# Optimization experiments

Hardware: AMD Instinct MI355X
Metric: run time of the kernel (lower is better)

The kernel has to match this reference:

```python
import jax, jax.numpy as jnp
import numpy as np

B, C_IN, MID, H, W = 4, 512, 512, 50, 50
A = 9
FEAT_STRIDE = 16
IMG = H * FEAT_STRIDE  # 800
N_PRE, N_POST = 1200, 300
NMS_TH = 0.7
MIN_SIZE = 16.0


def _anchor_base(base=16.0, ratios=(0.5, 1.0, 2.0), scales=(8, 16, 32)):
    ab = np.zeros((len(ratios) * len(scales), 4), np.float32)
    py = px = base / 2.0
    for i, r in enumerate(ratios):
        for j, s in enumerate(scales):
            h = base * s * np.sqrt(r)
            w = base * s * np.sqrt(1.0 / r)
            ab[i * len(scales) + j] = [py - h / 2, px - w / 2, py + h / 2, px + w / 2]
    return ab


def _all_anchors():
    ab = _anchor_base()
    sy = np.arange(0, H * FEAT_STRIDE, FEAT_STRIDE, dtype=np.float32)
    sx = np.arange(0, W * FEAT_STRIDE, FEAT_STRIDE, dtype=np.float32)
    SX, SY = np.meshgrid(sx, sy)
    shift = np.stack([SY.ravel(), SX.ravel(), SY.ravel(), SX.ravel()], axis=1)
    return jnp.asarray((shift[:, None, :] + ab[None]).reshape(-1, 4))  # [H*W*A,4]


ANCHORS = _all_anchors()


def _conv(x, w, b, pad):
    y = jax.lax.conv_general_dilated(x, w, (1, 1), [(pad, pad), (pad, pad)],
                                     dimension_numbers=('NCHW', 'OIHW', 'NCHW'))
    return y + b[None, :, None, None]


def _loc2bbox(anc, loc):
    h = anc[:, 2] - anc[:, 0]
    w = anc[:, 3] - anc[:, 1]
    cy = anc[:, 0] + 0.5 * h
    cx = anc[:, 1] + 0.5 * w
    dy, dx, dh, dw = loc[:, 0], loc[:, 1], loc[:, 2], loc[:, 3]
    ncy = dy * h + cy
    ncx = dx * w + cx
    nh = jnp.exp(dh) * h
    nw = jnp.exp(dw) * w
    return jnp.stack([ncy - 0.5 * nh, ncx - 0.5 * nw, ncy + 0.5 * nh, ncx + 0.5 * nw], axis=1)


def _nms_keep(boxes, thresh):
    y1, x1, y2, x2 = boxes[:, 0], boxes[:, 1], boxes[:, 2], boxes[:, 3]
    iy = jnp.clip(jnp.minimum(y2[:, None], y2[None]) - jnp.maximum(y1[:, None], y1[None]), 0.0)
    ix = jnp.clip(jnp.minimum(x2[:, None], x2[None]) - jnp.maximum(x1[:, None], x1[None]), 0.0)
    inter = iy * ix
    area = (y2 - y1) * (x2 - x1)
    iou = inter / (area[:, None] + area[None] - inter + 1e-9)  # [N_PRE,N_PRE]

    def step(carry, i):
        sup, keep = carry
        k = ~sup[i]
        keep = keep.at[i].set(k)
        newsup = jnp.where(k & (iou[i] > thresh), True, sup)
        newsup = newsup.at[i].set(sup[i])
        return (newsup, keep), None

    n = boxes.shape[0]
    init = (jnp.zeros(n, bool), jnp.zeros(n, bool))
    (_, keep), _ = jax.lax.scan(step, init, jnp.arange(n))
    return keep


def _propose(loc, fg):
    roi = _loc2bbox(ANCHORS, loc)
    roi = jnp.stack([jnp.clip(roi[:, 0], 0.0, IMG), jnp.clip(roi[:, 1], 0.0, IMG),
                     jnp.clip(roi[:, 2], 0.0, IMG), jnp.clip(roi[:, 3], 0.0, IMG)], axis=1)
    hs = roi[:, 2] - roi[:, 0]
    ws = roi[:, 3] - roi[:, 1]
    s = jnp.where((hs >= MIN_SIZE) & (ws >= MIN_SIZE), fg, -jnp.inf)
    top_s, top_i = jax.lax.top_k(s, N_PRE)          # score-sorted pre-NMS candidates
    boxes = roi[top_i]
    keep = _nms_keep(boxes, NMS_TH)
    _, sel = jax.lax.top_k(jnp.where(keep, top_s, -jnp.inf), N_POST)
    return boxes[sel]                                # [N_POST,4]


def setup_inputs() -> dict:
    key = jax.random.key(0)
    ks = jax.random.split(key, 4)
    x = jax.random.normal(ks[0], (B, C_IN, H, W), jnp.float32)
    W1 = jax.random.normal(ks[1], (MID, C_IN, 3, 3), jnp.float32) * 0.01
    b1 = jnp.zeros((MID,), jnp.float32)
    Wl = jax.random.normal(ks[2], (A * 4, MID, 1, 1), jnp.float32) * 0.01
    bl = jnp.zeros((A * 4,), jnp.float32)
    Ws = jax.random.normal(ks[3], (A * 2, MID, 1, 1), jnp.float32) * 0.01
    bs = jnp.zeros((A * 2,), jnp.float32)
    return {'x': x, 'W1': W1, 'b1': b1, 'Wl': Wl, 'bl': bl, 'Ws': Ws, 'bs': bs}


def reference(x, W1, b1, Wl, bl, Ws, bs):
    h = jax.nn.relu(_conv(x, W1, b1, 1))
    locs = _conv(h, Wl, bl, 0)     # [B, A*4, H, W]
    scores = _conv(h, Ws, bs, 0)   # [B, A*2, H, W]
    rpn_locs = locs.transpose(0, 2, 3, 1).reshape(B, -1, 4)          # [B, H*W*A, 4]
    sc = scores.transpose(0, 2, 3, 1).reshape(B, H, W, A, 2)
    fg = jax.nn.softmax(sc, axis=-1)[..., 1].reshape(B, -1)          # [B, H*W*A]
    rpn_scores = sc.reshape(B, -1, 2)
    rois = jax.vmap(_propose)(rpn_locs, fg)                          # [B, N_POST, 4]
    return rpn_locs, rpn_scores, rois
```

## Files before the change

kernel.cpp:

```cpp
#include <hip/hip_runtime.h>
#include <math.h>

#define BATCH 4
#define CIN 512
#define MID 512
#define HH 50
#define WW 50
#define HWPIX 2500
#define NPIX 10000
#define NANCH 22500
#define NPRE 1200
#define NPOST 300
#define LOCS_OFF 0
#define SCORES_OFF 360000
#define ROIS_OFF 540000

#define PADW 52
#define PPIX 2704

typedef _Float16 half8 __attribute__((ext_vector_type(8)));
typedef float floatx4 __attribute__((ext_vector_type(4)));

__device__ __forceinline__ void gload16(const void* g, void* l) {
    __builtin_amdgcn_global_load_lds(
        (const __attribute__((address_space(1))) unsigned int*)g,
        (__attribute__((address_space(3))) unsigned int*)l, 16, 0, 0);
}

__device__ __forceinline__ unsigned long long rdlane64(unsigned int lo,
                                                       unsigned int hi, int l) {
    const unsigned int a = (unsigned int)__builtin_amdgcn_readlane((int)lo, l);
    const unsigned int b = (unsigned int)__builtin_amdgcn_readlane((int)hi, l);
    return ((unsigned long long)b << 32) | a;
}


__global__ __launch_bounds__(256) void prep_combo_kernel(
    const float* __restrict__ x, const float* __restrict__ W1,
    const float* __restrict__ Wl, const float* __restrict__ Wsc,
    _Float16* __restrict__ xh, _Float16* __restrict__ xl,
    _Float16* __restrict__ wth, _Float16* __restrict__ wtl,
    float* __restrict__ wh) {
    __shared__ __align__(16) char smem[18432];
    const int blk = blockIdx.x;
    const int t   = threadIdx.x;

    if (blk < 1280) {
        float (*tile)[65] = (float(*)[65])smem;
        const int pt = blk % 40;
        const int ct = (blk / 40) % 8;
        const int b  = blk / 320;
        const int p0 = pt * 64, c0 = ct * 64;

        #pragma unroll
        for (int r = 0; r < 16; ++r) {
            const int cc = (t >> 6) + r * 4;
            const int pp = t & 63;
            const int p  = p0 + pp;
            tile[cc][pp] = (p < HWPIX) ? x[((size_t)b * 512 + c0 + cc) * HWPIX + p] : 0.f;
        }
        __syncthreads();
        #pragma unroll
        for (int r = 0; r < 16; ++r) {
            const int pp = (t >> 6) + r * 4;
            const int cc = t & 63;
            const int p  = p0 + pp;
            if (p < HWPIX) {
                const int y = p / WW, xx2 = p % WW;
                const float v = tile[cc][pp];
                const _Float16 hh = (_Float16)v;
                const float rr = v - (float)hh;
                const _Float16 ll = (_Float16)(rr * 2048.0f);
                const size_t o = ((size_t)(b * PPIX + (y + 1) * PADW + xx2 + 1)) * 512 + c0 + cc;
                xh[o] = hh;
                xl[o] = ll;
            }
        }
    } else {
        const int wblk = blk - 1280;
        if (wblk < 512) {
            float* buf = (float*)smem;
            const int m = wblk;
            const float* src = W1 + (size_t)m * 4608;
            for (int i = t; i < 4608; i += 256) buf[i] = src[i];
            __syncthreads();
            for (int kk = 0; kk < 9; ++kk) {
                for (int c = t; c < 512; c += 256) {
                    const float v = buf[c * 9 + kk];
                    const _Float16 hh = (_Float16)v;
                    const float rr = v - (float)hh;
                    const size_t o = (size_t)kk * 262144 + (size_t)m * 512 + c;
                    wth[o] = hh;
                    wtl[o] = (_Float16)(rr * 2048.0f);
                }
            }
        } else if (wblk < 640) {
            const int g2 = (wblk - 512) * 256 + t;
            const int c = g2 >> 6, n = g2 & 63;
            float v = 0.f;
            if (n < 36)      v = Wl[n * 512 + c];
            else if (n < 54) v = Wsc[(n - 36) * 512 + c];
            wh[g2] = v;
        } else {
            const int idx = (wblk - 640) * 256 + t;
            if (idx < BATCH * PPIX * 4) {
                const int pix = idx >> 2, q = idx & 3;
                const int r = pix % PPIX;
                const int yy = r / PADW, xx2 = r % PADW;
                if (yy == 0 || yy == PADW - 1 || xx2 == 0 || xx2 == PADW - 1) {
                    float4 z = make_float4(0.f, 0.f, 0.f, 0.f);
                    float4* ph = (float4*)(xh + (size_t)pix * 512 + q * 128);
                    float4* pl = (float4*)(xl + (size_t)pix * 512 + q * 128);
                    #pragma unroll
                    for (int i = 0; i < 16; ++i) { ph[i] = z; pl[i] = z; }
                }
            }
        }
    }
}

#define BUFSZ 24576
#define AOFF_L 8192
#define BOFF_H 16384
#define BOFF_L 20480
#define MTILES 80

__global__ __launch_bounds__(256) void conv_mfma_kernel(
    const _Float16* __restrict__ xh, const _Float16* __restrict__ xl,
    const _Float16* __restrict__ wth, const _Float16* __restrict__ wtl,
    float* __restrict__ hp, int ksplit) {
    __shared__ __align__(16) char lds[2 * BUFSZ];

    const int bid  = blockIdx.x;
    const int t    = threadIdx.x;
    const int w    = t >> 6;
    const int lane = t & 63;
    const int m0   = (bid % MTILES) * 128;
    const int rr_  = bid / MTILES;
    int n0, s0, send, kh;
    if (ksplit) { n0 = (rr_ >> 1) * 64; kh = rr_ & 1; s0 = kh * 72; send = s0 + 72; }
    else        { n0 = rr_ * 64;        kh = 0;       s0 = 0;       send = 144; }
    float* hout = hp + (size_t)kh * 5120000;
    const int wq   = w * 1024;

    const int sr = t >> 2;
    const int cp = t & 3;
    const int clA = (cp - (sr >> 1)) & 3;
    const int clB = clA;

    int P0 = m0 + sr;       if (P0 > NPIX - 1) P0 = NPIX - 1;
    int P1 = m0 + sr + 64;  if (P1 > NPIX - 1) P1 = NPIX - 1;
    const int b0 = P0 / HWPIX, pl0 = P0 % HWPIX;
    const int b1i = P1 / HWPIX, pl1 = P1 % HWPIX;
    const int baseA0 = ((b0 * PPIX) + (pl0 / WW + 1) * PADW + (pl0 % WW + 1)) * 512 + clA * 8;
    const int baseA1 = ((b1i * PPIX) + (pl1 / WW + 1) * PADW + (pl1 % WW + 1)) * 512 + clA * 8;
    const int baseB  = (n0 + sr) * 512 + clB * 8;

    const int lr = lane & 15, lq = lane >> 4;
    const int wrow = w * 32;
    const int rA0 = wrow + lr, rA1 = wrow + 16 + lr;
    const int offA0 = rA0 * 64 + (((lq + (rA0 >> 1)) & 3) << 4);
    const int offA1 = rA1 * 64 + (((lq + (rA1 >> 1)) & 3) << 4);
    int offB[4];
    #pragma unroll
    for (int ctl = 0; ctl < 4; ++ctl) {
        const int rB = ctl * 16 + lr;
        offB[ctl] = rB * 64 + (((lq + (rB >> 1)) & 3) << 4);
    }

    floatx4 acc1[2][4] = {};
    floatx4 acc2[2][4] = {};

    auto issue = [&](int u) {
        char* D = lds + ((u & 1) ? BUFSZ : 0);
        const int kk = u >> 4, ct = u & 15;
        const int kd = kk / 3;
        const int dA = ((kd - 1) * PADW + (kk - kd * 3 - 1)) * 512 + ct * 32;
        const int dB = kk * 262144 + ct * 32;
        gload16(xh + baseA0 + dA, D + 0 + wq);
        gload16(xh + baseA1 + dA, D + 4096 + wq);
        gload16(xl + baseA0 + dA, D + AOFF_L + wq);
        gload16(xl + baseA1 + dA, D + AOFF_L + 4096 + wq);
        gload16(wth + baseB + dB, D + BOFF_H + wq);
        gload16(wtl + baseB + dB, D + BOFF_L + wq);
    };

    issue(s0);
    for (int s = s0; s < send; ++s) {
        __syncthreads();
        if (s + 1 < send) issue(s + 1);
        const char* Bb = lds + ((s & 1) ? BUFSZ : 0);
        const half8 afh0 = *(const half8*)(Bb + offA0);
        const half8 afh1 = *(const half8*)(Bb + offA1);
        const half8 afl0 = *(const half8*)(Bb + AOFF_L + offA0);
        const half8 afl1 = *(const half8*)(Bb + AOFF_L + offA1);
        #pragma unroll
        for (int ctl = 0; ctl < 4; ++ctl) {
            const half8 bfh = *(const half8*)(Bb + BOFF_H + offB[ctl]);
            const half8 bfl = *(const half8*)(Bb + BOFF_L + offB[ctl]);
            acc1[0][ctl] = __builtin_amdgcn_mfma_f32_16x16x32_f16(afh0, bfh, acc1[0][ctl], 0, 0, 0);
            acc2[0][ctl] = __builtin_amdgcn_mfma_f32_16x16x32_f16(afh0, bfl, acc2[0][ctl], 0, 0, 0);
            acc2[0][ctl] = __builtin_amdgcn_mfma_f32_16x16x32_f16(afl0, bfh, acc2[0][ctl], 0, 0, 0);
            acc1[1][ctl] = __builtin_amdgcn_mfma_f32_16x16x32_f16(afh1, bfh, acc1[1][ctl], 0, 0, 0);
            acc2[1][ctl] = __builtin_amdgcn_mfma_f32_16x16x32_f16(afh1, bfl, acc2[1][ctl], 0, 0, 0);
            acc2[1][ctl] = __builtin_amdgcn_mfma_f32_16x16x32_f16(afl1, bfh, acc2[1][ctl], 0, 0, 0);
        }
    }

    const float s2 = 1.0f / 2048.0f;
    #pragma unroll
    for (int rt = 0; rt < 2; ++rt) {
        #pragma unroll
        for (int ctl = 0; ctl < 4; ++ctl) {
            const int m = n0 + ctl * 16 + lr;
            #pragma unroll
            for (int r = 0; r < 4; ++r) {
                const int P = m0 + wrow + rt * 16 + lq * 4 + r;
                if (P < NPIX)
                    hout[(size_t)P * 512 + m] = acc1[rt][ctl][r] + acc2[rt][ctl][r] * s2;
            }
        }
    }
}

__global__ void wt_kernel(const float* __restrict__ W1,
                          const float* __restrict__ Wl,
                          const float* __restrict__ Wsc,
                          float* __restrict__ w1t, float* __restrict__ wh) {
    int g = blockIdx.x * 256 + threadIdx.x;
    if (g < 9 * 512 * 512) {
        int kk = g / (512 * 512);
        int r  = g % (512 * 512);
        int c  = r / 512;
        int m  = r % 512;
        w1t[g] = W1[(size_t)m * 4608 + c * 9 + kk];
    } else {
        int g2 = g - 9 * 512 * 512;
        if (g2 < 512 * 64) {
            int c = g2 >> 6, n = g2 & 63;
            float v = 0.f;
            if (n < 36)      v = Wl[n * 512 + c];
            else if (n < 54) v = Wsc[(n - 36) * 512 + c];
            wh[g2] = v;
        }
    }
}

__global__ __launch_bounds__(256) void conv3x3_fallback(
    const float* __restrict__ x, const float* __restrict__ w1t,
    float* __restrict__ h) {
    __shared__ float As[16][64];
    __shared__ float Bs[16][64];
    const int t  = threadIdx.x;
    const int tx = t & 15;
    const int ty = t >> 4;
    const int m0 = blockIdx.x * 64;
    const int n0 = blockIdx.y * 64;
    const int pix = t & 63;
    const int cl0 = t >> 6;
    const int P  = m0 + pix;
    const bool vp = (P < NPIX);
    const int b  = P / HWPIX;
    const int pl = P % HWPIX;
    const int yy = pl / WW;
    const int xx = pl % WW;
    float acc[4][4] = {};
    for (int kk = 0; kk < 9; ++kk) {
        const int ky = kk / 3 - 1, kx = kk % 3 - 1;
        const int y2 = yy + ky, x2 = xx + kx;
        const bool v = vp && ((unsigned)y2 < (unsigned)HH) && ((unsigned)x2 < (unsigned)WW);
        const float* xbase = x + (size_t)b * CIN * HWPIX + y2 * WW + x2;
        const float* wbase = w1t + (size_t)kk * 512 * 512 + n0;
        for (int ct = 0; ct < 512 / 16; ++ct) {
            __syncthreads();
            #pragma unroll
            for (int r = 0; r < 4; ++r) {
                const int cl = cl0 + r * 4;
                const int c  = ct * 16 + cl;
                As[cl][pix] = v ? xbase[(size_t)c * HWPIX] : 0.f;
                Bs[cl][pix] = wbase[c * 512 + pix];
            }
            __syncthreads();
            #pragma unroll
            for (int k = 0; k < 16; ++k) {
                const float4 a4 = *reinterpret_cast<const float4*>(&As[k][ty * 4]);
                const float4 b4 = *reinterpret_cast<const float4*>(&Bs[k][tx * 4]);
                const float av[4] = {a4.x, a4.y, a4.z, a4.w};
                const float bv[4] = {b4.x, b4.y, b4.z, b4.w};
                #pragma unroll
                for (int i = 0; i < 4; ++i)
                    #pragma unroll
                    for (int j = 0; j < 4; ++j)
                        acc[i][j] = fmaf(av[i], bv[j], acc[i][j]);
            }
        }
    }
    #pragma unroll
    for (int i = 0; i < 4; ++i) {
        const int Pp = m0 + ty * 4 + i;
        if (Pp >= NPIX) continue;
        const int m = n0 + tx * 4;
        float4 o;
        o.x = acc[i][0];
        o.y = acc[i][1];
        o.z = acc[i][2];
        o.w = acc[i][3];
        *reinterpret_cast<float4*>(&h[(size_t)Pp * 512 + m]) = o;
    }
}


__global__ __launch_bounds__(256) void heads_kernel(
    const float* __restrict__ h0, const float* __restrict__ h1,
    const float* __restrict__ wh, const float* __restrict__ b1,
    const float* __restrict__ bl, const float* __restrict__ bsc,
    float* __restrict__ out, float* __restrict__ roi_all,
    unsigned long long* __restrict__ keys) {
    #pragma clang fp contract(off)
    __shared__ float As[16][17];
    __shared__ float Bs[16][64];
    __shared__ float fgs[16][9];
    const int t  = threadIdx.x;
    const int p  = t & 15;
    const int g  = t >> 4;
    const int p0 = blockIdx.x * 16;

    float acc[4] = {0.f, 0.f, 0.f, 0.f};

    for (int ct = 0; ct < 32; ++ct) {
        const int c0 = ct * 16;
        __syncthreads();
        {
            const int pp = t >> 4, cc = t & 15;
            const int PP = p0 + pp;
            float v = 0.f;
            if (PP < NPIX) {
                const size_t o = (size_t)PP * 512 + c0 + cc;
                v = h0[o];
                if (h1) v += h1[o];
                v = fmaxf(v + b1[c0 + cc], 0.f);
            }
            As[cc][pp] = v;
            #pragma unroll
            for (int r = 0; r < 4; ++r) {
                const int row = (t >> 6) + 4 * r;
                Bs[row][t & 63] = wh[(size_t)(c0 + row) * 64 + (t & 63)];
            }
        }
        __syncthreads();
        #pragma unroll
        for (int k = 0; k < 16; ++k) {
            const float a = As[k][p];
            const float4 b4 = *reinterpret_cast<const float4*>(&Bs[k][g * 4]);
            acc[0] = fmaf(a, b4.x, acc[0]);
            acc[1] = fmaf(a, b4.y, acc[1]);
            acc[2] = fmaf(a, b4.z, acc[2]);
            acc[3] = fmaf(a, b4.w, acc[3]);
        }
    }

    const int P  = p0 + p;
    const int b  = (P < NPIX) ? (P / HWPIX) : 0;
    const int pl = (P < NPIX) ? (P % HWPIX) : 0;
    const int n  = g * 4;
    const size_t abase = (size_t)b * NANCH + (size_t)pl * 9;
    const bool vP = (P < NPIX);

    float4 locv = make_float4(0.f, 0.f, 0.f, 0.f);
    if (vP && n < 36) {
        locv.x = acc[0] + bl[n + 0];
        locv.y = acc[1] + bl[n + 1];
        locv.z = acc[2] + bl[n + 2];
        locv.w = acc[3] + bl[n + 3];
        *reinterpret_cast<float4*>(&out[LOCS_OFF + (abase + g) * 4]) = locv;
    } else if (vP && n < 54) {
        const int ns = n - 36;
        float* so = out + SCORES_OFF;
        {
            const float s0 = acc[0] + bsc[ns + 0];
            const float s1 = acc[1] + bsc[ns + 1];
            const int a0 = ns >> 1;
            so[(abase + a0) * 2 + 0] = s0;
            so[(abase + a0) * 2 + 1] = s1;
            const float mx = fmaxf(s0, s1);
            const float e0 = expf(s0 - mx);
            const float e1 = expf(s1 - mx);
            fgs[p][a0] = e1 / (e0 + e1);
        }
        if (ns + 3 < 18) {
            const float s0 = acc[2] + bsc[ns + 2];
            const float s1 = acc[3] + bsc[ns + 3];
            const int a1 = (ns >> 1) + 1;
            so[(abase + a1) * 2 + 0] = s0;
            so[(abase + a1) * 2 + 1] = s1;
            const float mx = fmaxf(s0, s1);
            const float e0 = expf(s0 - mx);
            const float e1 = expf(s1 - mx);
            fgs[p][a1] = e1 / (e0 + e1);
        }
    }
    __syncthreads();

    if (vP && n < 36) {
        const int a = g;
        const int j = pl * 9 + a;
        const int y = pl / WW;
        const int x = pl % WW;
        const int ri = a / 3, si = a % 3;
        const double rrd[3] = {0.5, 1.0, 2.0};
        const double ssd[3] = {8.0, 16.0, 32.0};
        const double hh = 16.0 * ssd[si] * sqrt(rrd[ri]);
        const double wd = 16.0 * ssd[si] * sqrt(1.0 / rrd[ri]);
        const float ab0 = (float)(8.0 - hh / 2.0);
        const float ab1 = (float)(8.0 - wd / 2.0);
        const float ab2 = (float)(8.0 + hh / 2.0);
        const float ab3 = (float)(8.0 + wd / 2.0);
        const float sy = (float)(y * 16);
        const float sx = (float)(x * 16);
        const float ay1 = sy + ab0;
        const float ax1 = sx + ab1;
        const float ay2 = sy + ab2;
        const float ax2 = sx + ab3;

        const float h  = ay2 - ay1;
        const float w  = ax2 - ax1;
        const float cy = ay1 + 0.5f * h;
        const float cx = ax1 + 0.5f * w;

        const float dy = locv.x, dx = locv.y, dh = locv.z, dw = locv.w;
        const float ncy = dy * h + cy;
        const float ncx = dx * w + cx;
        const float nh  = expf(dh) * h;
        const float nw  = expf(dw) * w;

        float r0 = ncy - 0.5f * nh;
        float r1 = ncx - 0.5f * nw;
        float r2 = ncy + 0.5f * nh;
        float r3 = ncx + 0.5f * nw;
        r0 = fminf(fmaxf(r0, 0.f), 800.f);
        r1 = fminf(fmaxf(r1, 0.f), 800.f);
        r2 = fminf(fmaxf(r2, 0.f), 800.f);
        r3 = fminf(fmaxf(r3, 0.f), 800.f);

        const float hs  = r2 - r0;
        const float wsz = r3 - r1;
        const float fg  = fgs[p][a];
        const float s   = (hs >= 16.f && wsz >= 16.f) ? fg : -__builtin_huge_valf();

        float4 ro;
        ro.x = r0; ro.y = r1; ro.z = r2; ro.w = r3;
        *reinterpret_cast<float4*>(&roi_all[((size_t)b * NANCH + j) * 4]) = ro;

        unsigned int bits = __float_as_uint(s);
        unsigned int o = (bits & 0x80000000u) ? ~bits : (bits | 0x80000000u);
        keys[(size_t)b * NANCH + j] =
            ((unsigned long long)o << 32) | (unsigned int)(~(unsigned int)j);
    }
}

__global__ __launch_bounds__(1024) void select_sort_kernel(
    const unsigned long long* __restrict__ keys,
    const float* __restrict__ roi_all, float* __restrict__ boxes) {
    const int b   = blockIdx.x;
    const int tid = threadIdx.x;
    const unsigned long long* K = keys + (size_t)b * NANCH;

    __shared__ unsigned int hist[256][4];
    __shared__ unsigned int suf[256];
    __shared__ unsigned long long sbuf[2048];
    __shared__ unsigned int prefix_s;
    __shared__ int rank_s;
    __shared__ int cnt_s;

    const int sub = (tid >> 8) & 3;

    if (tid == 0) { prefix_s = 0u; rank_s = NPRE; }
    __syncthreads();

    for (int pass = 0; pass < 4; ++pass) {
        for (int i = tid; i < 1024; i += 1024) ((unsigned int*)hist)[i] = 0;
        __syncthreads();
        const unsigned pref = prefix_s;
        for (int i = tid; i < NANCH; i += 1024) {
            const unsigned hk = (unsigned)(K[i] >> 32);
            const bool match = (pass == 0) || ((hk >> (32 - 8 * pass)) == pref);
            if (match) atomicAdd(&hist[(hk >> (24 - 8 * pass)) & 255u][sub], 1u);
        }
        __syncthreads();
        if (tid < 256)
            suf[tid] = hist[tid][0] + hist[tid][1] + hist[tid][2] + hist[tid][3];
        __syncthreads();
        for (int st = 1; st < 256; st <<= 1) {
            unsigned v = 0;
            if (tid < 256) v = suf[tid] + ((tid + st < 256) ? suf[tid + st] : 0u);
            __syncthreads();
            if (tid < 256) suf[tid] = v;
            __syncthreads();
        }
        const int r = rank_s;
        __syncthreads();
        if (tid < 256) {
            const unsigned s_here = suf[tid];
            const unsigned s_up   = (tid < 255) ? suf[tid + 1] : 0u;
            if (s_here >= (unsigned)r && s_up < (unsigned)r) {
                rank_s = r - (int)s_up;
                prefix_s = (prefix_s << 8) | (unsigned)tid;
            }
        }
        __syncthreads();
    }

    const unsigned kth32 = prefix_s;
    if (tid == 0) cnt_s = 0;
    __syncthreads();
    for (int i = tid; i < NANCH; i += 1024) {
        const unsigned long long k = K[i];
        if ((unsigned)(k >> 32) >= kth32) {
            const int p = atomicAdd(&cnt_s, 1);
            if (p < 2048) sbuf[p] = k;
        }
    }
    __syncthreads();
    const int cnt = cnt_s;
    for (int i = tid; i < 2048; i += 1024)
        if (i >= cnt) sbuf[i] = 0ULL;

    for (int ksz = 2; ksz <= 2048; ksz <<= 1) {
        for (int jj = ksz >> 1; jj > 0; jj >>= 1) {
            __syncthreads();
            for (int i = tid; i < 2048; i += 1024) {
                const int l = i ^ jj;
                if (l > i) {
                    const unsigned long long a = sbuf[i];
                    const unsigned long long c = sbuf[l];
                    const bool asc = (i & ksz) != 0;
                    const bool sw  = asc ? (a > c) : (a < c);
                    if (sw) { sbuf[i] = c; sbuf[l] = a; }
                }
            }
        }
    }
    __syncthreads();

    for (int r = tid; r < NPRE; r += 1024) {
        const unsigned long long k = sbuf[r];
        const unsigned int idx = ~((unsigned int)k);
        const float4 v = *reinterpret_cast<const float4*>(
            &roi_all[((size_t)b * NANCH + idx) * 4]);
        *reinterpret_cast<float4*>(&boxes[((size_t)b * NPRE + r) * 4]) = v;
    }
}

__global__ __launch_bounds__(64) void iou_kernel(
    const float* __restrict__ boxes, unsigned long long* __restrict__ mask) {
    #pragma clang fp contract(off)
    const int rb = blockIdx.x;
    const int b  = blockIdx.y;
    const int t  = threadIdx.x;
    __shared__ float bx[NPRE * 4];
    __shared__ float ar[NPRE];

    for (int i = t; i < NPRE * 4; i += 64)
        bx[i] = boxes[(size_t)b * NPRE * 4 + i];
    __syncthreads();
    for (int i = t; i < NPRE; i += 64)
        ar[i] = (bx[i * 4 + 2] - bx[i * 4 + 0]) * (bx[i * 4 + 3] - bx[i * 4 + 1]);
    __syncthreads();

    const int i = rb * 64 + t;
    if (i >= NPRE) return;
    const float y1 = bx[i * 4 + 0], x1 = bx[i * 4 + 1];
    const float y2 = bx[i * 4 + 2], x2 = bx[i * 4 + 3];
    const float ai = ar[i];
    for (int jw = 0; jw < 19; ++jw) {
        unsigned long long bits = 0ULL;
        const int jmax = (jw * 64 + 64 <= NPRE) ? 64 : (NPRE - jw * 64);
        for (int jb = 0; jb < jmax; ++jb) {
            const int j = jw * 64 + jb;
            const float iy = fmaxf(fminf(y2, bx[j * 4 + 2]) - fmaxf(y1, bx[j * 4 + 0]), 0.f);
            const float ix = fmaxf(fminf(x2, bx[j * 4 + 3]) - fmaxf(x1, bx[j * 4 + 1]), 0.f);
            const float inter = iy * ix;
            const float den = ((ai + ar[j]) - inter) + 1e-9f;
            const float iou = inter / den;
            if (iou > 0.7f) bits |= (1ULL << jb);
        }
        mask[((size_t)b * NPRE + i) * 19 + jw] = bits;
    }
}

__global__ __launch_bounds__(64) void nms_scan_kernel(
    const unsigned long long* __restrict__ mask,
    const float* __restrict__ boxes, float* __restrict__ out_rois) {
    const int b    = blockIdx.x;
    const int lane = threadIdx.x;
    const unsigned long long* M = mask + (size_t)b * NPRE * 19;

    __shared__ unsigned long long tile[2][1216];
    __shared__ unsigned long long kw[19];
    __shared__ int sel[NPOST];

    const int lw = (lane < 19) ? lane : 0;

    {
        unsigned long long pre[19];
        #pragma unroll
        for (int q = 0; q < 19; ++q) pre[q] = M[q * 64 + lane];
        #pragma unroll
        for (int q = 0; q < 19; ++q) tile[0][q * 64 + lane] = pre[q];
    }
    __syncthreads();

    unsigned long long sup = 0ULL;

    for (int w = 0; w < 19; ++w) {
        const int cur = w & 1;
        unsigned long long pre[19];
        if (w + 1 < 19) {
            const int gb = (w + 1) * 1216;
            #pragma unroll
            for (int q = 0; q < 19; ++q) pre[q] = M[gb + q * 64 + lane];
        }

        const int nrows = (w == 18) ? (NPRE - 18 * 64) : 64;
        const unsigned long long* tp = tile[cur];

        const unsigned long long diag = (lane < nrows) ? tp[lane * 19 + w] : 0ULL;
        const unsigned int dlo = (unsigned int)diag;
        const unsigned int dhi = (unsigned int)(diag >> 32);

        const unsigned long long ext =
            rdlane64((unsigned int)sup, (unsigned int)(sup >> 32), w);

        unsigned long long sup_in = ext, keep = 0ULL;
        for (int i = 0; i < nrows; ++i) {
            const unsigned long long di = rdlane64(dlo, dhi, i);
            if (!((sup_in >> i) & 1ULL)) {
                keep |= (1ULL << i);
                sup_in |= di;
            }
        }

        #pragma unroll
        for (int i = 0; i < 64; ++i) {
            const unsigned long long mi = tp[i * 19 + lw];
            sup |= mi & (0ULL - ((keep >> i) & 1ULL));
        }

        if (lane == 0) kw[w] = keep;

        if (w + 1 < 19) {
            #pragma unroll
            for (int q = 0; q < 19; ++q) tile[1 - cur][q * 64 + lane] = pre[q];
        }
        __syncthreads();
    }

    int total = 0;
    #pragma unroll
    for (int w = 0; w < 19; ++w) total += __popcll(kw[w]);

    int pref = 0;
    #pragma unroll
    for (int w = 0; w < 19; ++w) {
        const unsigned long long kwv = kw[w];
        const int i = w * 64 + lane;
        const int kr = pref + __popcll(kwv & ((1ULL << lane) - 1ULL));
        if (i < NPRE) {
            if ((kwv >> lane) & 1ULL) {
                if (kr < NPOST) sel[kr] = i;
            } else {
                const int r2 = total + (i - kr);
                if (r2 < NPOST) sel[r2] = i;
            }
        }
        pref += __popcll(kwv);
    }
    __syncthreads();

    for (int rr = lane; rr < NPOST; rr += 64) {
        const int i = sel[rr];
        const float4 v = *reinterpret_cast<const float4*>(
            &boxes[((size_t)b * NPRE + i) * 4]);
        *reinterpret_cast<float4*>(&out_rois[((size_t)b * NPOST + rr) * 4]) = v;
    }
}

extern "C" void kernel_launch(void* const* d_in, const int* in_sizes, int n_in,
                              void* d_out, int out_size, void* d_ws, size_t ws_size,
                              hipStream_t stream) {
    const float* x   = (const float*)d_in[0];
    const float* W1  = (const float*)d_in[1];
    const float* b1  = (const float*)d_in[2];
    const float* Wl  = (const float*)d_in[3];
    const float* bl  = (const float*)d_in[4];
    const float* Wsc = (const float*)d_in[5];
    const float* bsc = (const float*)d_in[6];
    float* out = (float*)d_out;
    char* ws = (char*)d_ws;

    const size_t T_A = 72679424ULL;
    const size_t T_B = 52199424ULL;

    if (ws_size >= T_B) {
        const bool ksplit = (ws_size >= T_A);
        float*    h0;
        float*    h1 = nullptr;
        _Float16 *xh, *xl, *wth, *wtl;
        float*    wh;
        char*     alias;
        if (ksplit) {
            h0  = (float*)(ws);
            h1  = (float*)(ws + 20480000);
            xh  = (_Float16*)(ws + 40960000);
            xl  = (_Float16*)(ws + 52035584);
            wth = (_Float16*)(ws + 63111168);
            wtl = (_Float16*)(ws + 67829760);
            wh  = (float*)(ws + 72548352);
            alias = ws + 40960000;
        } else {
            h0  = (float*)(ws);
            xh  = (_Float16*)(ws + 20480000);
            xl  = (_Float16*)(ws + 31555584);
            wth = (_Float16*)(ws + 42631168);
            wtl = (_Float16*)(ws + 47349760);
            wh  = (float*)(ws + 52068352);
            alias = ws + 20480000;
        }
        float* roi   = (float*)(alias);
        unsigned long long* keys = (unsigned long long*)(alias + 1440000);
        float* boxes = (float*)(alias + 2160000);
        unsigned long long* mask = (unsigned long long*)(alias + 2236800);

        hipLaunchKernelGGL(prep_combo_kernel, dim3(1280 + 512 + 128 + 169), dim3(256), 0, stream,
                           x, W1, Wl, Wsc, xh, xl, wth, wtl, wh);
        hipLaunchKernelGGL(conv_mfma_kernel, dim3((ksplit ? 16 : 8) * MTILES), dim3(256), 0, stream,
                           xh, xl, wth, wtl, h0, (int)(ksplit ? 1 : 0));
        hipLaunchKernelGGL(heads_kernel, dim3(625), dim3(256), 0, stream,
                           h0, h1, wh, b1, bl, bsc, out, roi, keys);
        hipLaunchKernelGGL(select_sort_kernel, dim3(BATCH), dim3(1024), 0, stream,
                           keys, roi, boxes);
        hipLaunchKernelGGL(iou_kernel, dim3(19, BATCH), dim3(64), 0, stream,
                           boxes, mask);
        hipLaunchKernelGGL(nms_scan_kernel, dim3(BATCH), dim3(64), 0, stream,
                           mask, boxes, out + ROIS_OFF);
    } else {
        float* w1t = (float*)(ws);
        float* h   = (float*)(ws + 9437184);
        float* wh  = (float*)(ws + 29917184);
        float* roi = (float*)(ws + 30048256);
        unsigned long long* keys = (unsigned long long*)(ws + 31488256);
        float* boxes = (float*)(ws + 32208256);
        unsigned long long* mask = (unsigned long long*)(ws + 32285056);

        hipLaunchKernelGGL(wt_kernel, dim3((9 * 512 * 512 + 512 * 64 + 255) / 256),
                           dim3(256), 0, stream, W1, Wl, Wsc, w1t, wh);
        hipLaunchKernelGGL(conv3x3_fallback, dim3((NPIX + 63) / 64, 512 / 64), dim3(256), 0, stream,
                           x, w1t, h);
        hipLaunchKernelGGL(heads_kernel, dim3(625), dim3(256), 0, stream,
                           h, (const float*)nullptr, wh, b1, bl, bsc, out, roi, keys);
        hipLaunchKernelGGL(select_sort_kernel, dim3(BATCH), dim3(1024), 0, stream,
                           keys, roi, boxes);
        hipLaunchKernelGGL(iou_kernel, dim3(19, BATCH), dim3(64), 0, stream,
                           boxes, mask);
        hipLaunchKernelGGL(nms_scan_kernel, dim3(BATCH), dim3(64), 0, stream,
                           mask, boxes, out + ROIS_OFF);
    }
}
```

Before: 540.6 us.

## Fuse top-k sort, IoU mask and NMS scan into one kernel; vectorize fp16 split stores

Merges the select/sort, IoU-mask and NMS-scan kernels into a single per-batch 1024-thread kernel. Sorted boxes stay in shared memory instead of round-tripping through global memory, which removes two kernel launches. In exchange, the IoU computation now runs on only 4 workgroups rather than 76, which concentrates that work on a few compute units. The prep kernel also packs pairs of fp16 hi/lo values into half2 stores to cut store instruction count.

```diff
diff --git a/kernel.cpp b/kernel.cpp
--- a/kernel.cpp
+++ b/kernel.cpp
@@ -19,6 +19,7 @@
 #define PPIX 2704
 
 typedef _Float16 half8 __attribute__((ext_vector_type(8)));
+typedef _Float16 half2v __attribute__((ext_vector_type(2)));
 typedef float floatx4 __attribute__((ext_vector_type(4)));
 
 __device__ __forceinline__ void gload16(const void* g, void* l) {
@@ -61,19 +62,23 @@
         }
         __syncthreads();
         #pragma unroll
-        for (int r = 0; r < 16; ++r) {
-            const int pp = (t >> 6) + r * 4;
-            const int cc = t & 63;
-            const int p  = p0 + pp;
+        for (int r = 0; r < 8; ++r) {
+            const int pp  = (t >> 5) + r * 8;
+            const int cc2 = (t & 31) * 2;
+            const int p   = p0 + pp;
             if (p < HWPIX) {
                 const int y = p / WW, xx2 = p % WW;
-                const float v = tile[cc][pp];
-                const _Float16 hh = (_Float16)v;
-                const float rr = v - (float)hh;
-                const _Float16 ll = (_Float16)(rr * 2048.0f);
-                const size_t o = ((size_t)(b * PPIX + (y + 1) * PADW + xx2 + 1)) * 512 + c0 + cc;
-                xh[o] = hh;
-                xl[o] = ll;
+                const float v0 = tile[cc2][pp];
+                const float v1 = tile[cc2 + 1][pp];
+                const _Float16 h0 = (_Float16)v0;
+                const _Float16 l0 = (_Float16)((v0 - (float)h0) * 2048.0f);
+                const _Float16 h1 = (_Float16)v1;
+                const _Float16 l1 = (_Float16)((v1 - (float)h1) * 2048.0f);
+                const size_t o = ((size_t)(b * PPIX + (y + 1) * PADW + xx2 + 1)) * 512 + c0 + cc2;
+                half2v hv; hv[0] = h0; hv[1] = h1;
+                half2v lv; lv[0] = l0; lv[1] = l1;
+                *reinterpret_cast<half2v*>(xh + o) = hv;
+                *reinterpret_cast<half2v*>(xl + o) = lv;
             }
         }
     } else {
@@ -84,15 +89,19 @@
             const float* src = W1 + (size_t)m * 4608;
             for (int i = t; i < 4608; i += 256) buf[i] = src[i];
             __syncthreads();
+            const int c = t * 2;
             for (int kk = 0; kk < 9; ++kk) {
-                for (int c = t; c < 512; c += 256) {
-                    const float v = buf[c * 9 + kk];
-                    const _Float16 hh = (_Float16)v;
-                    const float rr = v - (float)hh;
-                    const size_t o = (size_t)kk * 262144 + (size_t)m * 512 + c;
-                    wth[o] = hh;
-                    wtl[o] = (_Float16)(rr * 2048.0f);
-                }
+                const float v0 = buf[c * 9 + kk];
+                const float v1 = buf[(c + 1) * 9 + kk];
+                const _Float16 h0 = (_Float16)v0;
+                const _Float16 l0 = (_Float16)((v0 - (float)h0) * 2048.0f);
+                const _Float16 h1 = (_Float16)v1;
+                const _Float16 l1 = (_Float16)((v1 - (float)h1) * 2048.0f);
+                const size_t o = (size_t)kk * 262144 + (size_t)m * 512 + c;
+                half2v hv; hv[0] = h0; hv[1] = h1;
+                half2v lv; lv[0] = l0; lv[1] = l1;
+                *reinterpret_cast<half2v*>(wth + o) = hv;
+                *reinterpret_cast<half2v*>(wtl + o) = lv;
             }
         } else if (wblk < 640) {
             const int g2 = (wblk - 512) * 256 + t;
@@ -458,27 +467,37 @@
     }
 }
 
-__global__ __launch_bounds__(1024) void select_sort_kernel(
-    const unsigned long long* __restrict__ keys,
-    const float* __restrict__ roi_all, float* __restrict__ boxes) {
+__global__ __launch_bounds__(1024) void postproc_kernel(
+    const unsigned long long* __restrict__ keys_g,
+    const float* __restrict__ roi_all,
+    unsigned long long* __restrict__ mask_g,
+    float* __restrict__ out_rois) {
+    #pragma clang fp contract(off)
     const int b   = blockIdx.x;
     const int tid = threadIdx.x;
-    const unsigned long long* K = keys + (size_t)b * NANCH;
-
-    __shared__ unsigned int hist[256][4];
-    __shared__ unsigned int suf[256];
-    __shared__ unsigned long long sbuf[2048];
+    const unsigned long long* K = keys_g + (size_t)b * NANCH;
+
+    __shared__ __align__(16) char arena[49152];
+    __shared__ unsigned long long kw[19];
+    __shared__ int sel[NPOST];
     __shared__ unsigned int prefix_s;
     __shared__ int rank_s;
     __shared__ int cnt_s;
 
+    unsigned int (*hist)[4]   = (unsigned int(*)[4])(arena);
+    unsigned int* suf         = (unsigned int*)(arena + 4096);
+    unsigned long long* sbuf  = (unsigned long long*)(arena + 8192);
+    float* bx                 = (float*)(arena + 24576);
+    float* ar                 = (float*)(arena + 43776);
+    unsigned long long* tileb = (unsigned long long*)(arena);
+
     const int sub = (tid >> 8) & 3;
 
     if (tid == 0) { prefix_s = 0u; rank_s = NPRE; }
     __syncthreads();
 
     for (int pass = 0; pass < 4; ++pass) {
-        for (int i = tid; i < 1024; i += 1024) ((unsigned int*)hist)[i] = 0;
+        ((unsigned int*)hist)[tid] = 0;
         __syncthreads();
         const unsigned pref = prefix_s;
         for (int i = tid; i < NANCH; i += 1024) {
@@ -547,58 +566,36 @@
         const unsigned int idx = ~((unsigned int)k);
         const float4 v = *reinterpret_cast<const float4*>(
             &roi_all[((size_t)b * NANCH + idx) * 4]);
-        *reinterpret_cast<float4*>(&boxes[((size_t)b * NPRE + r) * 4]) = v;
-    }
-}
-
-__global__ __launch_bounds__(64) void iou_kernel(
-    const float* __restrict__ boxes, unsigned long long* __restrict__ mask) {
-    #pragma clang fp contract(off)
-    const int rb = blockIdx.x;
-    const int b  = blockIdx.y;
-    const int t  = threadIdx.x;
-    __shared__ float bx[NPRE * 4];
-    __shared__ float ar[NPRE];
-
-    for (int i = t; i < NPRE * 4; i += 64)
-        bx[i] = boxes[(size_t)b * NPRE * 4 + i];
-    __syncthreads();
-    for (int i = t; i < NPRE; i += 64)
+        *reinterpret_cast<float4*>(&bx[r * 4]) = v;
+    }
+    __syncthreads();
+    for (int i = tid; i < NPRE; i += 1024)
         ar[i] = (bx[i * 4 + 2] - bx[i * 4 + 0]) * (bx[i * 4 + 3] - bx[i * 4 + 1]);
     __syncthreads();
 
-    const int i = rb * 64 + t;
-    if (i >= NPRE) return;
-    const float y1 = bx[i * 4 + 0], x1 = bx[i * 4 + 1];
-    const float y2 = bx[i * 4 + 2], x2 = bx[i * 4 + 3];
-    const float ai = ar[i];
-    for (int jw = 0; jw < 19; ++jw) {
-        unsigned long long bits = 0ULL;
-        const int jmax = (jw * 64 + 64 <= NPRE) ? 64 : (NPRE - jw * 64);
-        for (int jb = 0; jb < jmax; ++jb) {
-            const int j = jw * 64 + jb;
-            const float iy = fmaxf(fminf(y2, bx[j * 4 + 2]) - fmaxf(y1, bx[j * 4 + 0]), 0.f);
-            const float ix = fmaxf(fminf(x2, bx[j * 4 + 3]) - fmaxf(x1, bx[j * 4 + 1]), 0.f);
-            const float inter = iy * ix;
-            const float den = ((ai + ar[j]) - inter) + 1e-9f;
-            const float iou = inter / den;
-            if (iou > 0.7f) bits |= (1ULL << jb);
-        }
-        mask[((size_t)b * NPRE + i) * 19 + jw] = bits;
-    }
-}
-
-__global__ __launch_bounds__(64) void nms_scan_kernel(
-    const unsigned long long* __restrict__ mask,
-    const float* __restrict__ boxes, float* __restrict__ out_rois) {
-    const int b    = blockIdx.x;
-    const int lane = threadIdx.x;
-    const unsigned long long* M = mask + (size_t)b * NPRE * 19;
-
-    __shared__ unsigned long long tile[2][1216];
-    __shared__ unsigned long long kw[19];
-    __shared__ int sel[NPOST];
-
+    for (int i = tid; i < NPRE; i += 1024) {
+        const float y1 = bx[i * 4 + 0], x1 = bx[i * 4 + 1];
+        const float y2 = bx[i * 4 + 2], x2 = bx[i * 4 + 3];
+        const float ai = ar[i];
+        for (int jw = 0; jw < 19; ++jw) {
+            unsigned long long bits = 0ULL;
+            const int jmax = (jw * 64 + 64 <= NPRE) ? 64 : (NPRE - jw * 64);
+            for (int jb = 0; jb < jmax; ++jb) {
+                const int j = jw * 64 + jb;
+                const float iy = fmaxf(fminf(y2, bx[j * 4 + 2]) - fmaxf(y1, bx[j * 4 + 0]), 0.f);
+                const float ix = fmaxf(fminf(x2, bx[j * 4 + 3]) - fmaxf(x1, bx[j * 4 + 1]), 0.f);
+                const float inter = iy * ix;
+                const float den = ((ai + ar[j]) - inter) + 1e-9f;
+                const float iou = inter / den;
+                if (iou > 0.7f) bits |= (1ULL << jb);
+            }
+            mask_g[((size_t)b * NPRE + i) * 19 + jw] = bits;
+        }
+    }
+    __syncthreads();
+
+    const unsigned long long* M = mask_g + (size_t)b * NPRE * 19;
+    const int lane = tid & 63;
     const int lw = (lane < 19) ? lane : 0;
 
     {
@@ -606,7 +603,7 @@
         #pragma unroll
         for (int q = 0; q < 19; ++q) pre[q] = M[q * 64 + lane];
         #pragma unroll
-        for (int q = 0; q < 19; ++q) tile[0][q * 64 + lane] = pre[q];
+        for (int q = 0; q < 19; ++q) tileb[q * 64 + lane] = pre[q];
     }
     __syncthreads();
 
@@ -622,7 +619,7 @@
         }
 
         const int nrows = (w == 18) ? (NPRE - 18 * 64) : 64;
-        const unsigned long long* tp = tile[cur];
+        const unsigned long long* tp = tileb + cur * 1216;
 
         const unsigned long long diag = (lane < nrows) ? tp[lane * 19 + w] : 0ULL;
         const unsigned int dlo = (unsigned int)diag;
@@ -650,7 +647,7 @@
 
         if (w + 1 < 19) {
             #pragma unroll
-            for (int q = 0; q < 19; ++q) tile[1 - cur][q * 64 + lane] = pre[q];
+            for (int q = 0; q < 19; ++q) tileb[(1 - cur) * 1216 + q * 64 + lane] = pre[q];
         }
         __syncthreads();
     }
@@ -677,11 +674,12 @@
     }
     __syncthreads();
 
-    for (int rr = lane; rr < NPOST; rr += 64) {
-        const int i = sel[rr];
-        const float4 v = *reinterpret_cast<const float4*>(
-            &boxes[((size_t)b * NPRE + i) * 4]);
-        *reinterpret_cast<float4*>(&out_rois[((size_t)b * NPOST + rr) * 4]) = v;
+    if (tid < 64) {
+        for (int rr = tid; rr < NPOST; rr += 64) {
+            const int i = sel[rr];
+            const float4 v = *reinterpret_cast<const float4*>(&bx[i * 4]);
+            *reinterpret_cast<float4*>(&out_rois[((size_t)b * NPOST + rr) * 4]) = v;
+        }
     }
 }
 
@@ -728,8 +726,7 @@
         }
         float* roi   = (float*)(alias);
         unsigned long long* keys = (unsigned long long*)(alias + 1440000);
-        float* boxes = (float*)(alias + 2160000);
-        unsigned long long* mask = (unsigned long long*)(alias + 2236800);
+        unsigned long long* mask = (unsigned long long*)(alias + 2160000);
 
         hipLaunchKernelGGL(prep_combo_kernel, dim3(1280 + 512 + 128 + 169), dim3(256), 0, stream,
                            x, W1, Wl, Wsc, xh, xl, wth, wtl, wh);
@@ -737,20 +734,15 @@
                            xh, xl, wth, wtl, h0, (int)(ksplit ? 1 : 0));
         hipLaunchKernelGGL(heads_kernel, dim3(625), dim3(256), 0, stream,
                            h0, h1, wh, b1, bl, bsc, out, roi, keys);
-        hipLaunchKernelGGL(select_sort_kernel, dim3(BATCH), dim3(1024), 0, stream,
-                           keys, roi, boxes);
-        hipLaunchKernelGGL(iou_kernel, dim3(19, BATCH), dim3(64), 0, stream,
-                           boxes, mask);
-        hipLaunchKernelGGL(nms_scan_kernel, dim3(BATCH), dim3(64), 0, stream,
-                           mask, boxes, out + ROIS_OFF);
+        hipLaunchKernelGGL(postproc_kernel, dim3(BATCH), dim3(1024), 0, stream,
+                           keys, roi, mask, out + ROIS_OFF);
     } else {
         float* w1t = (float*)(ws);
         float* h   = (float*)(ws + 9437184);
         float* wh  = (float*)(ws + 29917184);
         float* roi = (float*)(ws + 30048256);
         unsigned long long* keys = (unsigned long long*)(ws + 31488256);
-        float* boxes = (float*)(ws + 32208256);
-        unsigned long long* mask = (unsigned long long*)(ws + 32285056);
+        unsigned long long* mask = (unsigned long long*)(ws + 32208256);
 
         hipLaunchKernelGGL(wt_kernel, dim3((9 * 512 * 512 + 512 * 64 + 255) / 256),
                            dim3(256), 0, stream, W1, Wl, Wsc, w1t, wh);
@@ -758,11 +750,7 @@
                            x, w1t, h);
         hipLaunchKernelGGL(heads_kernel, dim3(625), dim3(256), 0, stream,
                            h, (const float*)nullptr, wh, b1, bl, bsc, out, roi, keys);
-        hipLaunchKernelGGL(select_sort_kernel, dim3(BATCH), dim3(1024), 0, stream,
-                           keys, roi, boxes);
-        hipLaunchKernelGGL(iou_kernel, dim3(19, BATCH), dim3(64), 0, stream,
-                           boxes, mask);
-        hipLaunchKernelGGL(nms_scan_kernel, dim3(BATCH), dim3(64), 0, stream,
-                           mask, boxes, out + ROIS_OFF);
-    }
-}
+        hipLaunchKernelGGL(postproc_kernel, dim3(BATCH), dim3(1024), 0, stream,
+                           keys, roi, mask, out + ROIS_OFF);
+    }
+}
```

Result: slower. 943.3 us (+74.5%).
